# Performance work log

Measured on AMD Instinct MI355X. Metric: run time of the kernel, lower is better.

Reference implementation:

```python
import jax, jax.numpy as jnp
import numpy as np

BS, QLEN, DIM, NH = 4, 2048, 1024, 16
DH = DIM // NH
NEG = float(np.finfo(np.float32).min)


def setup_inputs() -> dict:
    key = jax.random.key(0)
    ks = jax.random.split(key, 10)
    s = 1.0 / np.sqrt(DIM)
    return {
        "hidden_states": jax.random.normal(ks[0], (BS, QLEN, DIM), jnp.float32),
        "attention_mask": jnp.ones((BS, QLEN), jnp.int32),
        "Wq": jax.random.normal(ks[1], (DIM, DIM), jnp.float32) * s,
        "bq": jnp.zeros((DIM,), jnp.float32),
        "Wk": jax.random.normal(ks[2], (DIM, DIM), jnp.float32) * s,
        "bk": jnp.zeros((DIM,), jnp.float32),
        "Wv": jax.random.normal(ks[3], (DIM, DIM), jnp.float32) * s,
        "bv": jnp.zeros((DIM,), jnp.float32),
        "Wo": jax.random.normal(ks[4], (DIM, DIM), jnp.float32) * s,
        "bo": jnp.zeros((DIM,), jnp.float32),
    }


def _heads(x, bs):
    # [bs, len, dim] -> [bs, n_heads, len, dim_per_head]
    return x.reshape(bs, -1, NH, DH).transpose(0, 2, 1, 3)


def reference(hidden_states, attention_mask, Wq, bq, Wk, bk, Wv, bv, Wo, bo):
    bs, qlen, dim = hidden_states.shape
    q = _heads(hidden_states @ Wq.T + bq, bs) / jnp.sqrt(jnp.asarray(DH, hidden_states.dtype))
    k = _heads(hidden_states @ Wk.T + bk, bs)
    v = _heads(hidden_states @ Wv.T + bv, bs)
    scores = jnp.einsum("bhqd,bhkd->bhqk", q, k)  # [bs, nh, qlen, klen]
    mask = (attention_mask == 0)[:, None, None, :]  # [bs,1,1,klen]
    scores = jnp.where(mask, NEG, scores)
    weights = jax.nn.softmax(scores.astype(jnp.float32), axis=-1).astype(scores.dtype)
    context = jnp.einsum("bhqk,bhkd->bhqd", weights, v)
    context = context.transpose(0, 2, 1, 3).reshape(bs, qlen, dim)
    return context @ Wo.T + bo
```

## Files before the change

### kernel.cpp

```cpp
#include <hip/hip_runtime.h>
#include <hip/hip_bf16.h>

#define BS 4
#define QLEN 2048
#define DIM 1024
#define NH 16
#define DH 64

typedef __attribute__((ext_vector_type(8))) short bf16x8;
typedef __attribute__((ext_vector_type(4))) float f32x4;
typedef unsigned short u16;
typedef unsigned int u32;
typedef unsigned long long u64;

__device__ __forceinline__ u32 cvtpk_bf16(float lo, float hi) {
    u32 r;
    asm("v_cvt_pk_bf16_f32 %0, %1, %2" : "=v"(r) : "v"(lo), "v"(hi));
    return r;
}
__device__ __forceinline__ u16 f2bf_hw(float f) { return (u16)cvtpk_bf16(f, f); }

__device__ __forceinline__ void async_lds16(const void* gp, void* lp) {
    __builtin_amdgcn_global_load_lds(
        (const __attribute__((address_space(1))) u32*)(u64)gp,
        (__attribute__((address_space(3))) u32*)(u32)(u64)lp,
        16, 0, 0);
}

__global__ void cvt_fused(const float* __restrict__ H,
                          const float* __restrict__ W0, const float* __restrict__ W1,
                          const float* __restrict__ W2, const float* __restrict__ W3,
                          u16* __restrict__ Hb,
                          u16* __restrict__ D0, u16* __restrict__ D1,
                          u16* __restrict__ D2, u16* __restrict__ D3) {
    const int h4 = (BS * QLEN * DIM) / 4;
    int i = blockIdx.x * blockDim.x + threadIdx.x;
    const float* s;
    u16* d;
    int off;
    if (i < h4) { s = H; d = Hb; off = i; }
    else {
        int j = i - h4;
        int ws = j >> 18;
        off = j & 262143;
        s = ws == 0 ? W0 : ws == 1 ? W1 : ws == 2 ? W2 : W3;
        d = ws == 0 ? D0 : ws == 1 ? D1 : ws == 2 ? D2 : D3;
    }
    float4 v = ((const float4*)s)[off];
    u32 lo = cvtpk_bf16(v.x, v.y), hi = cvtpk_bf16(v.z, v.w);
    uint2 o; o.x = lo; o.y = hi;
    ((uint2*)d)[off] = o;
}

__global__ __launch_bounds__(256) void gemm_qkv(
    const u16* __restrict__ Hb,
    const u16* __restrict__ Wq, const u16* __restrict__ Wk, const u16* __restrict__ Wv,
    const float* __restrict__ bq, const float* __restrict__ bk, const float* __restrict__ bvv,
    u16* __restrict__ Qb, u16* __restrict__ Kb, u16* __restrict__ Vt)
{
    __shared__ __align__(16) u16 As[128 * 32];
    __shared__ __align__(16) u16 Bs[128 * 32];
    const int z = blockIdx.z;
    const u16* W = z == 0 ? Wq : z == 1 ? Wk : Wv;
    const float* bias = z == 0 ? bq : z == 1 ? bk : bvv;
    const int t = threadIdx.x;
    const int w = t >> 6, lane = t & 63;
    const int lr = lane & 15, lg = lane >> 4;
    const int m0 = blockIdx.y * 128, n0 = blockIdx.x * 128;
    const int wm = (w >> 1) * 64, wn = (w & 1) * 64;
    const int srow = w * 16 + (lane >> 2);
    const int sk = (lane & 3) * 8;

    f32x4 acc[4][4] = {};

    for (int kt = 0; kt < DIM; kt += 32) {
        __syncthreads();
        async_lds16(Hb + (u64)(m0 + srow) * DIM + kt + sk,      &As[(w * 16) * 32]);
        async_lds16(Hb + (u64)(m0 + 64 + srow) * DIM + kt + sk, &As[(64 + w * 16) * 32]);
        async_lds16(W + (u64)(n0 + srow) * DIM + kt + sk,       &Bs[(w * 16) * 32]);
        async_lds16(W + (u64)(n0 + 64 + srow) * DIM + kt + sk,  &Bs[(64 + w * 16) * 32]);
        __syncthreads();
        bf16x8 a[4], b[4];
#pragma unroll
        for (int i = 0; i < 4; ++i) a[i] = *(const bf16x8*)&As[(wm + i * 16 + lr) * 32 + lg * 8];
#pragma unroll
        for (int i = 0; i < 4; ++i) b[i] = *(const bf16x8*)&Bs[(wn + i * 16 + lr) * 32 + lg * 8];
#pragma unroll
        for (int mi = 0; mi < 4; ++mi)
#pragma unroll
            for (int ni = 0; ni < 4; ++ni)
                acc[mi][ni] = __builtin_amdgcn_mfma_f32_16x16x32_bf16(a[mi], b[ni], acc[mi][ni], 0, 0, 0);
    }

#pragma unroll
    for (int mi = 0; mi < 4; ++mi)
#pragma unroll
        for (int ni = 0; ni < 4; ++ni) {
            const int col = n0 + wn + ni * 16 + lr;
            const float bb = bias[col];
#pragma unroll
            for (int r = 0; r < 4; ++r) {
                const int row = m0 + wm + mi * 16 + lg * 4 + r;
                const float v = acc[mi][ni][r] + bb;
                const int bh = (row >> 11) * NH + (col >> 6);
                const int q = row & (QLEN - 1);
                const int d = col & (DH - 1);
                if (z == 0)      Qb[((u64)bh * QLEN + q) * DH + d] = f2bf_hw(v * 0.125f);
                else if (z == 1) Kb[((u64)bh * QLEN + q) * DH + d] = f2bf_hw(v);
                else             Vt[((u64)bh * DH + d) * QLEN + q] = f2bf_hw(v);
            }
        }
}

__global__ __launch_bounds__(256) void gemm_o(
    const u16* __restrict__ A, const u16* __restrict__ W,
    const float* __restrict__ bias, float* __restrict__ ofp)
{
    __shared__ __align__(16) u16 As[128 * 32];
    __shared__ __align__(16) u16 Bs[128 * 32];
    const int t = threadIdx.x;
    const int w = t >> 6, lane = t & 63;
    const int lr = lane & 15, lg = lane >> 4;
    const int m0 = blockIdx.y * 128, n0 = blockIdx.x * 128;
    const int wm = (w >> 1) * 64, wn = (w & 1) * 64;
    const int srow = w * 16 + (lane >> 2);
    const int sk = (lane & 3) * 8;

    f32x4 acc[4][4] = {};

    for (int kt = 0; kt < DIM; kt += 32) {
        __syncthreads();
        async_lds16(A + (u64)(m0 + srow) * DIM + kt + sk,      &As[(w * 16) * 32]);
        async_lds16(A + (u64)(m0 + 64 + srow) * DIM + kt + sk, &As[(64 + w * 16) * 32]);
        async_lds16(W + (u64)(n0 + srow) * DIM + kt + sk,      &Bs[(w * 16) * 32]);
        async_lds16(W + (u64)(n0 + 64 + srow) * DIM + kt + sk, &Bs[(64 + w * 16) * 32]);
        __syncthreads();
        bf16x8 a[4], b[4];
#pragma unroll
        for (int i = 0; i < 4; ++i) a[i] = *(const bf16x8*)&As[(wm + i * 16 + lr) * 32 + lg * 8];
#pragma unroll
        for (int i = 0; i < 4; ++i) b[i] = *(const bf16x8*)&Bs[(wn + i * 16 + lr) * 32 + lg * 8];
#pragma unroll
        for (int mi = 0; mi < 4; ++mi)
#pragma unroll
            for (int ni = 0; ni < 4; ++ni)
                acc[mi][ni] = __builtin_amdgcn_mfma_f32_16x16x32_bf16(a[mi], b[ni], acc[mi][ni], 0, 0, 0);
    }

#pragma unroll
    for (int mi = 0; mi < 4; ++mi)
#pragma unroll
        for (int ni = 0; ni < 4; ++ni) {
            const int col = n0 + wn + ni * 16 + lr;
            const float bb = bias[col];
#pragma unroll
            for (int r = 0; r < 4; ++r) {
                const int row = m0 + wm + mi * 16 + lg * 4 + r;
                ofp[(u64)row * DIM + col] = acc[mi][ni][r] + bb;
            }
        }
}

__global__ __launch_bounds__(256) void attn_kernel(
    const u16* __restrict__ Qb, const u16* __restrict__ Kb, const u16* __restrict__ Vt,
    const int* __restrict__ mask, u16* __restrict__ ctx)
{
    __shared__ __align__(16) u16 Ks[2][64 * 64];
    __shared__ __align__(16) u16 Vs[2][64 * 64];
    __shared__ __align__(16) u16 Pl[4][32 * 72];

    const int t = threadIdx.x;
    const int w = t >> 6, lane = t & 63;
    const int lr = lane & 15, lg = lane >> 4;
    const int bh = blockIdx.y;
    const int b = bh >> 4, hh = bh & 15;
    const int q0 = blockIdx.x * 128;
    const u16* Kbh = Kb + (u64)bh * QLEN * DH;
    const u16* Vth = Vt + (u64)bh * DH * QLEN;
    const int* mb = mask + b * QLEN;

    bf16x8 aq[2][2];
#pragma unroll
    for (int qa = 0; qa < 2; ++qa)
#pragma unroll
        for (int kk = 0; kk < 2; ++kk)
            aq[qa][kk] = *(const bf16x8*)&Qb[((u64)bh * QLEN + q0 + w * 32 + qa * 16 + lr) * DH + kk * 32 + lg * 8];

    f32x4 o[2][4] = {};
    float m[2] = {-3.0e38f, -3.0e38f};
    float lsum[2] = {0.f, 0.f};

    const int srow = lane >> 3;
    const int schunk = lane & 7;

#define STAGE(BUF, KT) do {                                                            \
    _Pragma("unroll")                                                                  \
    for (int c = 0; c < 2; ++c) {                                                      \
        const int row_ = c * 32 + w * 8 + srow;                                        \
        const int ch_ = schunk ^ (row_ & 7);                                           \
        async_lds16(Kbh + (u64)((KT) + row_) * DH + ch_ * 8, &Ks[BUF][(c * 32 + w * 8) * 64]); \
        async_lds16(Vth + (u64)row_ * QLEN + (KT) + ch_ * 8, &Vs[BUF][(c * 32 + w * 8) * 64]); \
    } } while (0)

    STAGE(0, 0);
    __syncthreads();

    int buf = 0;
    for (int kt = 0; kt < QLEN; kt += 64) {
        if (kt + 64 < QLEN) STAGE(buf ^ 1, kt + 64);

        f32x4 s[2][4] = {};
#pragma unroll
        for (int nf = 0; nf < 4; ++nf) {
            const int row = nf * 16 + lr;
#pragma unroll
            for (int kk = 0; kk < 2; ++kk) {
                const u32 off = ((u32)(row * 128 + kk * 64 + lg * 16)) ^ ((u32)(row & 7) << 4);
                bf16x8 ak = *(const bf16x8*)((const char*)&Ks[buf][0] + off);
                s[0][nf] = __builtin_amdgcn_mfma_f32_16x16x32_bf16(ak, aq[0][kk], s[0][nf], 0, 0, 0);
                s[1][nf] = __builtin_amdgcn_mfma_f32_16x16x32_bf16(ak, aq[1][kk], s[1][nf], 0, 0, 0);
            }
        }

        int4 mv[4];
#pragma unroll
        for (int nf = 0; nf < 4; ++nf) mv[nf] = *(const int4*)&mb[kt + nf * 16 + lg * 4];

#pragma unroll
        for (int qa = 0; qa < 2; ++qa) {
            float tm = s[qa][0][0];
#pragma unroll
            for (int nf = 0; nf < 4; ++nf)
#pragma unroll
                for (int r = 0; r < 4; ++r) tm = fmaxf(tm, s[qa][nf][r]);
            tm = fmaxf(tm, __shfl_xor(tm, 16));
            tm = fmaxf(tm, __shfl_xor(tm, 32));

            if (!__all(tm <= m[qa] + 8.0f)) {
                const float nm = fmaxf(m[qa], tm);
                const float corr = __expf(m[qa] - nm);
                m[qa] = nm;
                lsum[qa] *= corr;
#pragma unroll
                for (int r = 0; r < 4; ++r) {
                    const float cT = __shfl(corr, lg * 4 + r);
#pragma unroll
                    for (int nf2 = 0; nf2 < 4; ++nf2) o[qa][nf2][r] *= cT;
                }
            }

            float ps = 0.f;
#pragma unroll
            for (int nf = 0; nf < 4; ++nf) {
                float p[4];
#pragma unroll
                for (int r = 0; r < 4; ++r) {
                    const int mvr = r == 0 ? mv[nf].x : r == 1 ? mv[nf].y : r == 2 ? mv[nf].z : mv[nf].w;
                    const float e = __expf(s[qa][nf][r] - m[qa]);
                    p[r] = mvr ? e : 0.f;
                    ps += p[r];
                }
                uint2 pk;
                pk.x = cvtpk_bf16(p[0], p[1]);
                pk.y = cvtpk_bf16(p[2], p[3]);
                *(uint2*)&Pl[w][(qa * 16 + lr) * 72 + nf * 16 + lg * 4] = pk;
            }
            lsum[qa] += ps;
        }

        bf16x8 ap[2][2];
#pragma unroll
        for (int qa = 0; qa < 2; ++qa)
#pragma unroll
            for (int kk = 0; kk < 2; ++kk)
                ap[qa][kk] = *(const bf16x8*)&Pl[w][(qa * 16 + lr) * 72 + kk * 32 + lg * 8];

#pragma unroll
        for (int nf2 = 0; nf2 < 4; ++nf2) {
            const int row = nf2 * 16 + lr;
#pragma unroll
            for (int kk = 0; kk < 2; ++kk) {
                const u32 off = ((u32)(row * 128 + kk * 64 + lg * 16)) ^ ((u32)(row & 7) << 4);
                bf16x8 bv = *(const bf16x8*)((const char*)&Vs[buf][0] + off);
                o[0][nf2] = __builtin_amdgcn_mfma_f32_16x16x32_bf16(ap[0][kk], bv, o[0][nf2], 0, 0, 0);
                o[1][nf2] = __builtin_amdgcn_mfma_f32_16x16x32_bf16(ap[1][kk], bv, o[1][nf2], 0, 0, 0);
            }
        }

        __syncthreads();
        buf ^= 1;
    }

#pragma unroll
    for (int qa = 0; qa < 2; ++qa) {
        float l = lsum[qa];
        l += __shfl_xor(l, 16);
        l += __shfl_xor(l, 32);
        const float inv = 1.0f / fmaxf(l, 1e-37f);
#pragma unroll
        for (int r = 0; r < 4; ++r) {
            const float iT = __shfl(inv, lg * 4 + r);
            const int q = q0 + w * 32 + qa * 16 + lg * 4 + r;
#pragma unroll
            for (int nf2 = 0; nf2 < 4; ++nf2) {
                const int d = nf2 * 16 + lr;
                ctx[(((u64)b * QLEN + q) * NH + hh) * DH + d] = f2bf_hw(o[qa][nf2][r] * iT);
            }
        }
    }
#undef STAGE
}

extern "C" void kernel_launch(void* const* d_in, const int* in_sizes, int n_in,
                              void* d_out, int out_size, void* d_ws, size_t ws_size,
                              hipStream_t stream) {
    const float* H    = (const float*)d_in[0];
    const int*   mask = (const int*)d_in[1];
    const float* Wq   = (const float*)d_in[2];
    const float* bq   = (const float*)d_in[3];
    const float* Wk   = (const float*)d_in[4];
    const float* bk   = (const float*)d_in[5];
    const float* Wv   = (const float*)d_in[6];
    const float* bv   = (const float*)d_in[7];
    const float* Wo   = (const float*)d_in[8];
    const float* bo   = (const float*)d_in[9];
    float* out = (float*)d_out;

    const u64 NTOK = (u64)BS * QLEN;
    const u64 HN = NTOK * DIM;
    const u64 WN = (u64)DIM * DIM;

    u16* Hb  = (u16*)d_ws;
    u16* Wqb = Hb + HN;
    u16* Wkb = Wqb + WN;
    u16* Wvb = Wkb + WN;
    u16* Wob = Wvb + WN;
    u16* Qb  = Wob + WN;
    u16* Kb  = Qb + HN;
    u16* Vtg = Kb + HN;
    u16* Ctx = Vtg + HN;

    cvt_fused<<<12288, 256, 0, stream>>>(H, Wq, Wk, Wv, Wo, Hb, Wqb, Wkb, Wvb, Wob);

    gemm_qkv<<<dim3(DIM / 128, (int)(NTOK / 128), 3), 256, 0, stream>>>(
        Hb, Wqb, Wkb, Wvb, bq, bk, bv, Qb, Kb, Vtg);

    attn_kernel<<<dim3(QLEN / 128, BS * NH), 256, 0, stream>>>(Qb, Kb, Vtg, mask, Ctx);

    gemm_o<<<dim3(DIM / 128, (int)(NTOK / 128)), 256, 0, stream>>>(Ctx, Wob, bo, out);
}
```

Measured before the change: 255.3 us.

## Rewrite attention with 32x32 MFMA, register-resident P, exp2 softmax and mask flags

The attention kernel moves from 16x16x32 to 32x32x16 bf16 MFMAs and computes S transposed so that P can be handed to the PV MFMA via permlane32_swap instead of a round trip through LDS. Softmax now uses exp2 with log2e folded into the Q scaling in the QKV GEMM, and rescales on every tile instead of conditionally. A new mask_prep kernel builds a float mask plus per-64-key flags, so masking is skipped for tiles with no masked keys. Blocks are also remapped so that consecutive ids spread across heads, which may change L2 locality. The cost is one extra small kernel launch and higher register pressure from the f32x16 accumulators.

```diff
diff --git a/kernel.cpp b/kernel.cpp
--- a/kernel.cpp
+++ b/kernel.cpp
@@ -9,9 +9,14 @@
 
 typedef __attribute__((ext_vector_type(8))) short bf16x8;
 typedef __attribute__((ext_vector_type(4))) float f32x4;
+typedef __attribute__((ext_vector_type(16))) float f32x16;
+typedef __attribute__((ext_vector_type(2))) unsigned int u32x2;
+typedef __attribute__((ext_vector_type(4))) unsigned int u32x4;
 typedef unsigned short u16;
 typedef unsigned int u32;
 typedef unsigned long long u64;
+
+#define LOG2E 1.44269504088896f
 
 __device__ __forceinline__ u32 cvtpk_bf16(float lo, float hi) {
     u32 r;
@@ -47,9 +52,21 @@
         d = ws == 0 ? D0 : ws == 1 ? D1 : ws == 2 ? D2 : D3;
     }
     float4 v = ((const float4*)s)[off];
-    u32 lo = cvtpk_bf16(v.x, v.y), hi = cvtpk_bf16(v.z, v.w);
-    uint2 o; o.x = lo; o.y = hi;
+    uint2 o;
+    o.x = cvtpk_bf16(v.x, v.y);
+    o.y = cvtpk_bf16(v.z, v.w);
     ((uint2*)d)[off] = o;
+}
+
+__global__ void mask_prep(const int* __restrict__ mask, float* __restrict__ maskF,
+                          int* __restrict__ flags) {
+    const int tile = blockIdx.x;
+    const int lane = threadIdx.x;
+    const int idx = tile * 64 + lane;
+    const int v = mask[idx];
+    maskF[idx] = v ? 1.0f : 0.0f;
+    u64 bal = __ballot(v == 0);
+    if (lane == 0) flags[tile] = (bal != 0ull) ? 1 : 0;
 }
 
 __global__ __launch_bounds__(256) void gemm_qkv(
@@ -105,7 +122,7 @@
                 const int bh = (row >> 11) * NH + (col >> 6);
                 const int q = row & (QLEN - 1);
                 const int d = col & (DH - 1);
-                if (z == 0)      Qb[((u64)bh * QLEN + q) * DH + d] = f2bf_hw(v * 0.125f);
+                if (z == 0)      Qb[((u64)bh * QLEN + q) * DH + d] = f2bf_hw(v * (0.125f * LOG2E));
                 else if (z == 1) Kb[((u64)bh * QLEN + q) * DH + d] = f2bf_hw(v);
                 else             Vt[((u64)bh * DH + d) * QLEN + q] = f2bf_hw(v);
             }
@@ -163,43 +180,43 @@
 
 __global__ __launch_bounds__(256) void attn_kernel(
     const u16* __restrict__ Qb, const u16* __restrict__ Kb, const u16* __restrict__ Vt,
-    const int* __restrict__ mask, u16* __restrict__ ctx)
+    const float* __restrict__ maskF, const int* __restrict__ mflags, u16* __restrict__ ctx)
 {
     __shared__ __align__(16) u16 Ks[2][64 * 64];
     __shared__ __align__(16) u16 Vs[2][64 * 64];
-    __shared__ __align__(16) u16 Pl[4][32 * 72];
 
     const int t = threadIdx.x;
     const int w = t >> 6, lane = t & 63;
-    const int lr = lane & 15, lg = lane >> 4;
-    const int bh = blockIdx.y;
+    const int l5 = lane & 31, hi = lane >> 5, l7 = lane & 7;
+
+    const int id = blockIdx.x + 16 * blockIdx.y;
+    const int v = (id & 7) * 128 + (id >> 3);
+    const int qt = v & 15, bh = v >> 4;
     const int b = bh >> 4, hh = bh & 15;
-    const int q0 = blockIdx.x * 128;
+    const int q0 = qt * 128;
+
     const u16* Kbh = Kb + (u64)bh * QLEN * DH;
     const u16* Vth = Vt + (u64)bh * DH * QLEN;
-    const int* mb = mask + b * QLEN;
-
-    bf16x8 aq[2][2];
-#pragma unroll
-    for (int qa = 0; qa < 2; ++qa)
-#pragma unroll
-        for (int kk = 0; kk < 2; ++kk)
-            aq[qa][kk] = *(const bf16x8*)&Qb[((u64)bh * QLEN + q0 + w * 32 + qa * 16 + lr) * DH + kk * 32 + lg * 8];
-
-    f32x4 o[2][4] = {};
-    float m[2] = {-3.0e38f, -3.0e38f};
-    float lsum[2] = {0.f, 0.f};
-
-    const int srow = lane >> 3;
-    const int schunk = lane & 7;
+    const float* mFb = maskF + b * QLEN;
+    const int* flb = mflags + b * (QLEN / 64);
+
+    const u16* qp = Qb + ((u64)bh * QLEN + q0 + w * 32 + l5) * DH + hi * 8;
+    bf16x8 bq[4];
+#pragma unroll
+    for (int dc = 0; dc < 4; ++dc) bq[dc] = *(const bf16x8*)(qp + dc * 16);
+
+    f32x16 o[2] = {};
+    float mrun = -3.0e38f, lsum = 0.f;
+
+    const int srow = lane >> 3, schunk = lane & 7;
 
 #define STAGE(BUF, KT) do {                                                            \
     _Pragma("unroll")                                                                  \
     for (int c = 0; c < 2; ++c) {                                                      \
-        const int row_ = c * 32 + w * 8 + srow;                                        \
+        const int row_ = w * 16 + c * 8 + srow;                                        \
         const int ch_ = schunk ^ (row_ & 7);                                           \
-        async_lds16(Kbh + (u64)((KT) + row_) * DH + ch_ * 8, &Ks[BUF][(c * 32 + w * 8) * 64]); \
-        async_lds16(Vth + (u64)row_ * QLEN + (KT) + ch_ * 8, &Vs[BUF][(c * 32 + w * 8) * 64]); \
+        async_lds16(Kbh + (u64)((KT) + row_) * DH + ch_ * 8, &Ks[BUF][(w * 16 + c * 8) * 64]); \
+        async_lds16(Vth + (u64)row_ * QLEN + (KT) + ch_ * 8, &Vs[BUF][(w * 16 + c * 8) * 64]); \
     } } while (0)
 
     STAGE(0, 0);
@@ -209,106 +226,105 @@
     for (int kt = 0; kt < QLEN; kt += 64) {
         if (kt + 64 < QLEN) STAGE(buf ^ 1, kt + 64);
 
-        f32x4 s[2][4] = {};
-#pragma unroll
-        for (int nf = 0; nf < 4; ++nf) {
-            const int row = nf * 16 + lr;
-#pragma unroll
-            for (int kk = 0; kk < 2; ++kk) {
-                const u32 off = ((u32)(row * 128 + kk * 64 + lg * 16)) ^ ((u32)(row & 7) << 4);
-                bf16x8 ak = *(const bf16x8*)((const char*)&Ks[buf][0] + off);
-                s[0][nf] = __builtin_amdgcn_mfma_f32_16x16x32_bf16(ak, aq[0][kk], s[0][nf], 0, 0, 0);
-                s[1][nf] = __builtin_amdgcn_mfma_f32_16x16x32_bf16(ak, aq[1][kk], s[1][nf], 0, 0, 0);
-            }
-        }
-
-        int4 mv[4];
-#pragma unroll
-        for (int nf = 0; nf < 4; ++nf) mv[nf] = *(const int4*)&mb[kt + nf * 16 + lg * 4];
-
-#pragma unroll
-        for (int qa = 0; qa < 2; ++qa) {
-            float tm = s[qa][0][0];
-#pragma unroll
-            for (int nf = 0; nf < 4; ++nf)
-#pragma unroll
-                for (int r = 0; r < 4; ++r) tm = fmaxf(tm, s[qa][nf][r]);
-            tm = fmaxf(tm, __shfl_xor(tm, 16));
-            tm = fmaxf(tm, __shfl_xor(tm, 32));
-
-            if (!__all(tm <= m[qa] + 8.0f)) {
-                const float nm = fmaxf(m[qa], tm);
-                const float corr = __expf(m[qa] - nm);
-                m[qa] = nm;
-                lsum[qa] *= corr;
-#pragma unroll
-                for (int r = 0; r < 4; ++r) {
-                    const float cT = __shfl(corr, lg * 4 + r);
-#pragma unroll
-                    for (int nf2 = 0; nf2 < 4; ++nf2) o[qa][nf2][r] *= cT;
+        const char* Kbase = (const char*)&Ks[buf][0];
+        const char* Vbase = (const char*)&Vs[buf][0];
+
+        f32x16 s[2] = {};
+#pragma unroll
+        for (int dc = 0; dc < 4; ++dc) {
+            const u32 off = (u32)(l5 * 128) + (u32)(((2 * dc + hi) ^ l7) << 4);
+            bf16x8 ak0 = *(const bf16x8*)(Kbase + off);
+            bf16x8 ak1 = *(const bf16x8*)(Kbase + off + 4096);
+            s[0] = __builtin_amdgcn_mfma_f32_32x32x16_bf16(ak0, bq[dc], s[0], 0, 0, 0);
+            s[1] = __builtin_amdgcn_mfma_f32_32x32x16_bf16(ak1, bq[dc], s[1], 0, 0, 0);
+        }
+
+        float mx[16];
+#pragma unroll
+        for (int i = 0; i < 16; ++i) mx[i] = fmaxf(s[0][i], s[1][i]);
+#pragma unroll
+        for (int st = 8; st > 0; st >>= 1)
+#pragma unroll
+            for (int i = 0; i < 16; ++i) if (i < st) mx[i] = fmaxf(mx[i], mx[i + st]);
+        const float tma = fmaxf(mx[0], __shfl_xor(mx[0], 32));
+
+        const float nm = fmaxf(mrun, tma);
+        const float corr = exp2f(mrun - nm);
+        mrun = nm;
+        lsum *= corr;
+#pragma unroll
+        for (int i = 0; i < 16; ++i) { o[0][i] *= corr; o[1][i] *= corr; }
+
+#pragma unroll
+        for (int i = 0; i < 16; ++i) {
+            s[0][i] = exp2f(s[0][i] - mrun);
+            s[1][i] = exp2f(s[1][i] - mrun);
+        }
+
+        if (flb[kt >> 6]) {
+#pragma unroll
+            for (int kb = 0; kb < 2; ++kb)
+#pragma unroll
+                for (int m = 0; m < 4; ++m) {
+                    float4 mm = *(const float4*)&mFb[kt + kb * 32 + m * 8 + hi * 4];
+                    s[kb][4 * m + 0] *= mm.x;
+                    s[kb][4 * m + 1] *= mm.y;
+                    s[kb][4 * m + 2] *= mm.z;
+                    s[kb][4 * m + 3] *= mm.w;
                 }
-            }
-
-            float ps = 0.f;
-#pragma unroll
-            for (int nf = 0; nf < 4; ++nf) {
-                float p[4];
-#pragma unroll
-                for (int r = 0; r < 4; ++r) {
-                    const int mvr = r == 0 ? mv[nf].x : r == 1 ? mv[nf].y : r == 2 ? mv[nf].z : mv[nf].w;
-                    const float e = __expf(s[qa][nf][r] - m[qa]);
-                    p[r] = mvr ? e : 0.f;
-                    ps += p[r];
-                }
-                uint2 pk;
-                pk.x = cvtpk_bf16(p[0], p[1]);
-                pk.y = cvtpk_bf16(p[2], p[3]);
-                *(uint2*)&Pl[w][(qa * 16 + lr) * 72 + nf * 16 + lg * 4] = pk;
-            }
-            lsum[qa] += ps;
-        }
-
-        bf16x8 ap[2][2];
-#pragma unroll
-        for (int qa = 0; qa < 2; ++qa)
-#pragma unroll
-            for (int kk = 0; kk < 2; ++kk)
-                ap[qa][kk] = *(const bf16x8*)&Pl[w][(qa * 16 + lr) * 72 + kk * 32 + lg * 8];
-
-#pragma unroll
-        for (int nf2 = 0; nf2 < 4; ++nf2) {
-            const int row = nf2 * 16 + lr;
-#pragma unroll
-            for (int kk = 0; kk < 2; ++kk) {
-                const u32 off = ((u32)(row * 128 + kk * 64 + lg * 16)) ^ ((u32)(row & 7) << 4);
-                bf16x8 bv = *(const bf16x8*)((const char*)&Vs[buf][0] + off);
-                o[0][nf2] = __builtin_amdgcn_mfma_f32_16x16x32_bf16(ap[0][kk], bv, o[0][nf2], 0, 0, 0);
-                o[1][nf2] = __builtin_amdgcn_mfma_f32_16x16x32_bf16(ap[1][kk], bv, o[1][nf2], 0, 0, 0);
-            }
+        }
+
+        {
+            float ps[16];
+#pragma unroll
+            for (int i = 0; i < 16; ++i) ps[i] = s[0][i] + s[1][i];
+#pragma unroll
+            for (int st = 8; st > 0; st >>= 1)
+#pragma unroll
+                for (int i = 0; i < 16; ++i) if (i < st) ps[i] += ps[i + st];
+            lsum += ps[0];
+        }
+
+#pragma unroll
+        for (int kc = 0; kc < 4; ++kc) {
+            const int kb = kc >> 1;
+            const int base = 8 * (kc & 1);
+            const u32 P00 = cvtpk_bf16(s[kb][base + 0], s[kb][base + 1]);
+            const u32 P01 = cvtpk_bf16(s[kb][base + 2], s[kb][base + 3]);
+            const u32 P10 = cvtpk_bf16(s[kb][base + 4], s[kb][base + 5]);
+            const u32 P11 = cvtpk_bf16(s[kb][base + 6], s[kb][base + 7]);
+            u32x2 w02 = __builtin_amdgcn_permlane32_swap(P00, P10, false, false);
+            u32x2 w13 = __builtin_amdgcn_permlane32_swap(P01, P11, false, false);
+            u32x4 words;
+            words.x = w02[0]; words.y = w13[0]; words.z = w02[1]; words.w = w13[1];
+            const bf16x8 bp = __builtin_bit_cast(bf16x8, words);
+
+            const u32 voff = (u32)(l5 * 128) + (u32)(((2 * kc + hi) ^ l7) << 4);
+            bf16x8 av0 = *(const bf16x8*)(Vbase + voff);
+            bf16x8 av1 = *(const bf16x8*)(Vbase + voff + 4096);
+            o[0] = __builtin_amdgcn_mfma_f32_32x32x16_bf16(av0, bp, o[0], 0, 0, 0);
+            o[1] = __builtin_amdgcn_mfma_f32_32x32x16_bf16(av1, bp, o[1], 0, 0, 0);
         }
 
         __syncthreads();
         buf ^= 1;
     }
-
-#pragma unroll
-    for (int qa = 0; qa < 2; ++qa) {
-        float l = lsum[qa];
-        l += __shfl_xor(l, 16);
-        l += __shfl_xor(l, 32);
-        const float inv = 1.0f / fmaxf(l, 1e-37f);
-#pragma unroll
-        for (int r = 0; r < 4; ++r) {
-            const float iT = __shfl(inv, lg * 4 + r);
-            const int q = q0 + w * 32 + qa * 16 + lg * 4 + r;
-#pragma unroll
-            for (int nf2 = 0; nf2 < 4; ++nf2) {
-                const int d = nf2 * 16 + lr;
-                ctx[(((u64)b * QLEN + q) * NH + hh) * DH + d] = f2bf_hw(o[qa][nf2][r] * iT);
-            }
-        }
-    }
 #undef STAGE
+
+    const float lall = lsum + __shfl_xor(lsum, 32);
+    const float inv = 1.0f / fmaxf(lall, 1e-37f);
+
+    u16* cp = ctx + (((u64)b * QLEN + (q0 + w * 32 + l5)) * NH + hh) * DH;
+#pragma unroll
+    for (int db = 0; db < 2; ++db)
+#pragma unroll
+        for (int m = 0; m < 4; ++m) {
+            const int d0 = db * 32 + m * 8 + hi * 4;
+            const u32 wA = cvtpk_bf16(o[db][4 * m + 0] * inv, o[db][4 * m + 1] * inv);
+            const u32 wB = cvtpk_bf16(o[db][4 * m + 2] * inv, o[db][4 * m + 3] * inv);
+            *(u32*)(cp + d0) = wA;
+            *(u32*)(cp + d0 + 2) = wB;
+        }
 }
 
 extern "C" void kernel_launch(void* const* d_in, const int* in_sizes, int n_in,
@@ -339,13 +355,16 @@
     u16* Kb  = Qb + HN;
     u16* Vtg = Kb + HN;
     u16* Ctx = Vtg + HN;
+    float* maskF = (float*)(Ctx + HN);
+    int* mflags = (int*)(maskF + BS * QLEN);
 
     cvt_fused<<<12288, 256, 0, stream>>>(H, Wq, Wk, Wv, Wo, Hb, Wqb, Wkb, Wvb, Wob);
+    mask_prep<<<BS * (QLEN / 64), 64, 0, stream>>>(mask, maskF, mflags);
 
     gemm_qkv<<<dim3(DIM / 128, (int)(NTOK / 128), 3), 256, 0, stream>>>(
         Hb, Wqb, Wkb, Wvb, bq, bk, bv, Qb, Kb, Vtg);
 
-    attn_kernel<<<dim3(QLEN / 128, BS * NH), 256, 0, stream>>>(Qb, Kb, Vtg, mask, Ctx);
+    attn_kernel<<<dim3(QLEN / 128, BS * NH), 256, 0, stream>>>(Qb, Kb, Vtg, maskF, mflags, Ctx);
 
     gemm_o<<<dim3(DIM / 128, (int)(NTOK / 128)), 256, 0, stream>>>(Ctx, Wob, bo, out);
 }
```

Measured after the change: 269.5 us. 1.06x slower.
